# Kernel tuning notes

Hardware: AMD Instinct MI355X
Metric: run time of the kernel (lower is better)

## Reference

```python
import jax, jax.numpy as jnp
import numpy as np


def setup_inputs() -> dict:
    key = jax.random.key(0)
    k1, k2 = jax.random.split(key)
    B, D, H, W = 32, 64, 32, 32
    K = 1024
    z_e = jax.random.normal(k1, (B, D, H, W), dtype=jnp.float32)
    # original init: uniform(-1/K, 1/K); use same scale
    emb = jax.random.uniform(k2, (K, D), dtype=jnp.float32, minval=-1.0 / K, maxval=1.0 / K)
    return {"z_e": z_e, "emb": emb}


COMMITMENT_COST = 0.25


def reference(z_e, emb):
    # z_e: [B, D, H, W], emb: [K, D]
    B, D, H, W = z_e.shape
    K = emb.shape[0]
    z = jnp.transpose(z_e, (0, 2, 3, 1))           # [B, H, W, D]
    flat = z.reshape(-1, D)                        # [N, D]
    N = flat.shape[0]

    dist = (
        jnp.sum(flat * flat, axis=1, keepdims=True)
        + jnp.sum(emb * emb, axis=1)
        - 2.0 * flat @ emb.T
    )
    idx = jnp.argmin(dist, axis=1)                 # [N]
    encodings = jax.nn.one_hot(idx, K, dtype=flat.dtype)  # [N, K]
    z_q = (encodings @ emb).reshape(z.shape)       # [B, H, W, D]

    e_latent_loss = jnp.mean((jax.lax.stop_gradient(z_q) - z) ** 2)
    q_latent_loss = jnp.mean((z_q - jax.lax.stop_gradient(z)) ** 2)
    loss = q_latent_loss + COMMITMENT_COST * e_latent_loss

    # straight-through estimator
    z_st = z + jax.lax.stop_gradient(z_q - z)

    avg_probs = jnp.sum(encodings, axis=0) / jnp.float32(N)
    perplexity = jnp.exp(-jnp.sum(avg_probs * jnp.log(avg_probs + 1e-10)))

    return (jnp.transpose(z_st, (0, 3, 1, 2)), loss, perplexity, encodings)
```

## Files before the change

### kernel.cpp

```cpp
#include <hip/hip_runtime.h>
#include <stdint.h>
#include <math.h>

constexpr int Kk  = 1024;

constexpr int OUT0_N   = 32 * 64 * 1024;
constexpr int OUT_LOSS = OUT0_N;
constexpr int OUT_PERP = OUT0_N + 1;
constexpr int OUT_ENC  = OUT0_N + 2;

constexpr size_t WS_CNT = 0;
constexpr size_t WS_LP  = 4096;
constexpr size_t WS_MBN = 12288;
constexpr size_t WS_KEY = 16384;

typedef short bf16x8 __attribute__((ext_vector_type(8)));
typedef float f32x16 __attribute__((ext_vector_type(16)));

__device__ __forceinline__ float norm64v(const float4* __restrict__ p) {
#pragma clang fp contract(off)
    float tt[64];
#pragma unroll
    for (int q = 0; q < 16; ++q) {
        float4 v = p[q];
        tt[4 * q + 0] = v.x * v.x;
        tt[4 * q + 1] = v.y * v.y;
        tt[4 * q + 2] = v.z * v.z;
        tt[4 * q + 3] = v.w * v.w;
    }
    float r[8];
#pragma unroll
    for (int j = 0; j < 8; ++j) r[j] = tt[j];
#pragma unroll
    for (int i = 8; i < 64; i += 8)
#pragma unroll
        for (int j = 0; j < 8; ++j) r[j] += tt[i + j];
    return ((r[0] + r[1]) + (r[2] + r[3])) + ((r[4] + r[5]) + (r[6] + r[7]));
}

__device__ __forceinline__ uint32_t fsort(float f) {
    uint32_t b = __float_as_uint(f);
    return (b & 0x80000000u) ? ~b : (b | 0x80000000u);
}

__device__ __forceinline__ unsigned short f2bf(float f) {
    uint32_t u = __float_as_uint(f);
    uint32_t r = (u + 0x7fffu + ((u >> 16) & 1u)) >> 16;
    return (unsigned short)r;
}

__device__ __forceinline__ unsigned long long
exact_key(float A, const float* __restrict__ xr, const float* __restrict__ emb,
          uint32_t code) {
    const float* er = emb + (size_t)code * 64;
    float C = 0.f;
#pragma unroll
    for (int d = 0; d < 64; ++d) C = __builtin_fmaf(xr[d], er[d], C);
    float Bv = norm64v((const float4*)er);
    float s = A + Bv;
    float dist = __builtin_fmaf(-2.f, C, s);
    return ((unsigned long long)fsort(dist) << 32) | code;
}

__global__ __launch_bounds__(256, 4)
void dist_mfma(const float* __restrict__ z_e, const float* __restrict__ emb,
               unsigned long long* __restrict__ lockey,
               uint32_t* __restrict__ counts,
               float* __restrict__ maxbn,
               float* __restrict__ out) {
    __shared__ unsigned short xbf[128 * 64];
    __shared__ unsigned short ebf[128 * 64];
    __shared__ float Bn_s[128];
    __shared__ float xsqp[2][128];
    __shared__ float mbn_s;
    const int t = threadIdx.x, lane = t & 63, wv = t >> 6, g = lane >> 5;
    const int rg = blockIdx.x >> 3, cg = blockIdx.x & 7;
    const int n0 = rg * 128, b = n0 >> 10, hw0 = n0 & 1023;
    const float* zb = z_e + (size_t)b * 65536 + hw0;

    {
        int hwi = t & 127, d4g = t >> 7;
        float xq = 0.f;
#pragma unroll
        for (int it = 0; it < 8; ++it) {
            int dbase = (d4g + it * 2) * 4;
            float v0 = zb[(size_t)(dbase + 0) * 1024 + hwi];
            float v1 = zb[(size_t)(dbase + 1) * 1024 + hwi];
            float v2 = zb[(size_t)(dbase + 2) * 1024 + hwi];
            float v3 = zb[(size_t)(dbase + 3) * 1024 + hwi];
            xq = __builtin_fmaf(v0, v0, xq);
            xq = __builtin_fmaf(v1, v1, xq);
            xq = __builtin_fmaf(v2, v2, xq);
            xq = __builtin_fmaf(v3, v3, xq);
            ushort4 bv;
            bv.x = f2bf(v0); bv.y = f2bf(v1); bv.z = f2bf(v2); bv.w = f2bf(v3);
            *(ushort4*)((char*)xbf + hwi * 128 + ((dbase * 2) ^ ((hwi & 7) << 4))) = bv;
        }
        xsqp[d4g][hwi] = xq;
    }
    {
        const float4* ep = (const float4*)(emb + (size_t)cg * 8192);
#pragma unroll
        for (int it = 0; it < 8; ++it) {
            int j = t + it * 256;
            float4 v = ep[j];
            int code = j >> 4, q = j & 15;
            ushort4 bv;
            bv.x = f2bf(v.x); bv.y = f2bf(v.y); bv.z = f2bf(v.z); bv.w = f2bf(v.w);
            *(ushort4*)((char*)ebf + code * 128 + ((q * 8) ^ ((code & 7) << 4))) = bv;
        }
    }
    if (t < 128) Bn_s[t] = norm64v((const float4*)(emb + (size_t)(cg * 128 + t) * 64));
    if (blockIdx.x == 0) ((uint4*)counts)[t] = make_uint4(0u, 0u, 0u, 0u);
    __syncthreads();
    if (wv == 0) {
        float m = fmaxf(Bn_s[lane], Bn_s[lane + 64]);
#pragma unroll
        for (int s = 1; s < 64; s <<= 1) m = fmaxf(m, __shfl_xor(m, s, 64));
        if (lane == 0) { mbn_s = m; if (rg == 0) maxbn[cg] = m; }
    }
    __syncthreads();

    const int rowl = wv * 32 + (lane & 31);
    const float xsq = xsqp[0][rowl] + xsqp[1][rowl];
    const float margin = 0.017f * sqrtf(xsq * mbn_s) + 1.0e-4f;

    const int swz = (lane & 7) << 4;
    bf16x8 bfr[4];
    const char* xb = (const char*)xbf + rowl * 128;
#pragma unroll
    for (int s = 0; s < 4; ++s)
        bfr[s] = *(const bf16x8*)(xb + ((s * 32 + g * 16) ^ swz));
    const char* ebase = (const char*)ebf + (lane & 31) * 128;

    float4* encz = (float4*)(out + OUT_ENC) + (size_t)blockIdx.x * 4096;
    const float4 zero4 = make_float4(0.f, 0.f, 0.f, 0.f);

    float runmin = 3.4e38f;
#pragma unroll 1
    for (int tm = 0; tm < 4; ++tm) {
        encz[(size_t)(tm * 2 + 0) * 256 + t] = zero4;
        encz[(size_t)(tm * 2 + 1) * 256 + t] = zero4;
        const char* p = ebase + tm * 4096;
        f32x16 acc = {};
#pragma unroll
        for (int s = 0; s < 4; ++s)
            acc = __builtin_amdgcn_mfma_f32_32x32x16_bf16(
                *(const bf16x8*)(p + ((s * 32 + g * 16) ^ swz)), bfr[s], acc, 0, 0, 0);
#pragma unroll
        for (int r = 0; r < 16; ++r) {
            int cl = tm * 32 + (r & 3) + 8 * (r >> 2) + 4 * g;
            runmin = fminf(runmin, __builtin_fmaf(-2.f, acc[r], Bn_s[cl]));
        }
    }
    runmin = fminf(runmin, __shfl_xor(runmin, 32, 64));
    const float thr = runmin + margin;

    uint32_t cnt = 0, c0 = 0, c1 = 0, c2 = 0;
#pragma unroll 1
    for (int tm = 0; tm < 4; ++tm) {
        encz[(size_t)(8 + tm * 2 + 0) * 256 + t] = zero4;
        encz[(size_t)(8 + tm * 2 + 1) * 256 + t] = zero4;
        const char* p = ebase + tm * 4096;
        f32x16 acc = {};
#pragma unroll
        for (int s = 0; s < 4; ++s)
            acc = __builtin_amdgcn_mfma_f32_32x32x16_bf16(
                *(const bf16x8*)(p + ((s * 32 + g * 16) ^ swz)), bfr[s], acc, 0, 0, 0);
#pragma unroll
        for (int r = 0; r < 16; ++r) {
            int cl = tm * 32 + (r & 3) + 8 * (r >> 2) + 4 * g;
            float sv = __builtin_fmaf(-2.f, acc[r], Bn_s[cl]);
            if (sv <= thr) {
                uint32_t gc = (uint32_t)(cg * 128 + cl);
                if (cnt == 0u) c0 = gc; else if (cnt == 1u) c1 = gc; else if (cnt == 2u) c2 = gc;
                ++cnt;
            }
        }
    }
    uint32_t pc = __shfl_xor(cnt, 32, 64);
    uint32_t p0 = __shfl_xor(c0, 32, 64);
    uint32_t p1 = __shfl_xor(c1, 32, 64);
    uint32_t p2 = __shfl_xor(c2, 32, 64);
    if (lane < 32) {
        uint32_t tot = cnt + pc;
        uint32_t lo;
        if (tot > 3u || tot == 0u) {
            lo = 3u << 30;
        } else {
            uint32_t a0 = c0, a1 = c1, a2 = c2;
            if (cnt == 0u)      { a0 = p0; a1 = p1; a2 = p2; }
            else if (cnt == 1u) { a1 = p0; a2 = p1; }
            else if (cnt == 2u) { a2 = p0; }
            if (tot < 2u) a1 = 0u;
            if (tot < 3u) a2 = 0u;
            lo = ((tot - 1u) << 30) | (a0 & 1023u) | ((a1 & 1023u) << 10) | ((a2 & 1023u) << 20);
        }
        unsigned long long key = ((unsigned long long)__float_as_uint(runmin) << 32) | lo;
        lockey[(size_t)(n0 + rowl) * 8 + cg] = key;
    }
}

__global__ __launch_bounds__(256)
void finish_kernel(const float* __restrict__ z_e,
                   const float* __restrict__ emb,
                   const unsigned long long* __restrict__ lockey,
                   const float* __restrict__ maxbn,
                   uint32_t* __restrict__ counts,
                   double* __restrict__ lp,
                   float* __restrict__ out) {
    __shared__ float zs[32 * 68];
    __shared__ float arow[32];
    __shared__ uint32_t scode[32];
    __shared__ uint8_t ncarr[32];
    __shared__ unsigned long long pkey[32][6];
    __shared__ uint32_t pairbuf[192];
    __shared__ uint32_t ovfbuf[32];
    __shared__ uint32_t npairs, novf;
    __shared__ float mbg_s;
    __shared__ unsigned long long rbuf[4];
    __shared__ double lred[4];
    const int t = threadIdx.x, lane = t & 63, wv = t >> 6;
    const int n0 = blockIdx.x * 32;
    const int b = n0 >> 10, hw0 = n0 & 1023;
    const int hwi = t & 31, dg = t >> 5;
    const size_t base = (size_t)b * 65536 + (size_t)(dg * 8) * 1024 + hw0 + hwi;

    if (t == 0) {
        npairs = 0u; novf = 0u;
        float mb = maxbn[0];
#pragma unroll
        for (int i = 1; i < 8; ++i) mb = fmaxf(mb, maxbn[i]);
        mbg_s = mb;
    }

    float zreg[8];
#pragma unroll
    for (int k = 0; k < 8; ++k) zreg[k] = z_e[base + (size_t)k * 1024];
#pragma unroll
    for (int m = 0; m < 2; ++m)
        *(float4*)&zs[hwi * 68 + dg * 8 + 4 * m] =
            make_float4(zreg[4 * m], zreg[4 * m + 1], zreg[4 * m + 2], zreg[4 * m + 3]);
    __syncthreads();

    if (t < 32) {
        const unsigned long long* k8 = lockey + (size_t)(n0 + t) * 8;
        unsigned long long kws[8];
#pragma unroll
        for (int i = 0; i < 8; ++i) kws[i] = k8[i];
        float gmin = 3.4e38f;
#pragma unroll
        for (int i = 0; i < 8; ++i)
            gmin = fminf(gmin, __uint_as_float((uint32_t)(kws[i] >> 32)));
        float A = norm64v((const float4*)&zs[t * 68]);
        arow[t] = A;
        const float thr = gmin + 0.017f * sqrtf(A * mbg_s) + 1.0e-4f;

        int nc = 0; uint32_t cand[6]; bool ovf = false;
#pragma unroll
        for (int i = 0; i < 8; ++i) {
            float f = __uint_as_float((uint32_t)(kws[i] >> 32));
            if (f > thr) continue;
            uint32_t lo = (uint32_t)kws[i], cc = lo >> 30;
            if (cc == 3u) { ovf = true; }
            else {
#pragma unroll
                for (uint32_t q = 0; q < 3u; ++q)
                    if (q <= cc) {
                        if (nc < 6) cand[nc] = (lo >> (10u * q)) & 1023u;
                        ++nc;
                    }
            }
        }
        if (ovf || nc > 6 || nc == 0) {
            ncarr[t] = 255u;
            ovfbuf[atomicAdd(&novf, 1u)] = (uint32_t)t;
        } else if (nc == 1) {
            ncarr[t] = 1u;
            scode[t] = cand[0];
        } else {
            ncarr[t] = (uint8_t)nc;
            uint32_t bs = atomicAdd(&npairs, (uint32_t)nc);
#pragma unroll
            for (int q = 0; q < 6; ++q)
                if (q < nc)
                    pairbuf[bs + q] = ((uint32_t)t << 13) | ((uint32_t)q << 10) | cand[q];
        }
    }
    __syncthreads();

    for (uint32_t p = t; p < npairs; p += 256u) {
        uint32_t pk = pairbuf[p];
        int row = (int)(pk >> 13), slot = (int)((pk >> 10) & 7u);
        pkey[row][slot] = exact_key(arow[row], &zs[row * 68], emb, pk & 1023u);
    }
    __syncthreads();

    for (uint32_t o = 0; o < novf; ++o) {
        int row = (int)ovfbuf[o];
        const float* xr = &zs[row * 68];
        float A = arow[row];
        unsigned long long best = ~0ULL;
#pragma unroll 1
        for (int cq = 0; cq < 4; ++cq) {
            unsigned long long key = exact_key(A, xr, emb, (uint32_t)(t + cq * 256));
            best = (key < best) ? key : best;
        }
#pragma unroll
        for (int m = 1; m < 64; m <<= 1) {
            unsigned long long ok = __shfl_xor(best, m, 64);
            best = (ok < best) ? ok : best;
        }
        if (lane == 0) rbuf[wv] = best;
        __syncthreads();
        if (t == 0) {
            unsigned long long bb = rbuf[0];
#pragma unroll
            for (int w = 1; w < 4; ++w) bb = (rbuf[w] < bb) ? rbuf[w] : bb;
            scode[row] = (uint32_t)bb;
        }
        __syncthreads();
    }

    if (t < 32) {
        uint8_t nc = ncarr[t];
        if (nc >= 2u && nc != 255u) {
            unsigned long long bb = pkey[t][0];
#pragma unroll
            for (int q = 1; q < 6; ++q)
                if (q < (int)nc && pkey[t][q] < bb) bb = pkey[t][q];
            scode[t] = (uint32_t)bb;
        }
    }
    __syncthreads();

    if (t < 32) {
        uint32_t code = scode[t];
        atomicAdd(&counts[code], 1u);
        out[(size_t)OUT_ENC + (size_t)(n0 + t) * 1024 + code] = 1.0f;
    }

    {
        const uint32_t code = scode[hwi];
        const float4* er4 = (const float4*)(emb + (size_t)code * 64) + dg * 2;
        double ls = 0.0;
#pragma unroll
        for (int k4 = 0; k4 < 2; ++k4) {
            float4 e4 = er4[k4];
            float f0 = e4.x, f1 = e4.y, f2 = e4.z, f3 = e4.w;
            size_t off = base + (size_t)(k4 * 4) * 1024;
            {
                float z = zreg[k4 * 4 + 0]; float tt = f0 - z;
                out[off] = z + tt;              ls += (double)tt * (double)tt;
            }
            {
                float z = zreg[k4 * 4 + 1]; float tt = f1 - z;
                out[off + 1024] = z + tt;       ls += (double)tt * (double)tt;
            }
            {
                float z = zreg[k4 * 4 + 2]; float tt = f2 - z;
                out[off + 2048] = z + tt;       ls += (double)tt * (double)tt;
            }
            {
                float z = zreg[k4 * 4 + 3]; float tt = f3 - z;
                out[off + 3072] = z + tt;       ls += (double)tt * (double)tt;
            }
        }
#pragma unroll
        for (int m = 32; m >= 1; m >>= 1) ls += __shfl_down(ls, m, 64);
        if ((t & 63) == 0) lred[t >> 6] = ls;
    }
    __syncthreads();
    if (t == 0) lp[blockIdx.x] = lred[0] + lred[1] + lred[2] + lred[3];
}

__global__ void scalar_kernel(const uint32_t* __restrict__ counts,
                              const double* __restrict__ lp,
                              float* __restrict__ out) {
    __shared__ double redl[4], redh[4];
    const int t = threadIdx.x;
    double ls = 0.0;
    for (int i = t; i < 1024; i += 256) ls += lp[i];
    double h = 0.0;
    for (int i = t; i < Kk; i += 256) {
        double p = (double)counts[i] * (1.0 / 32768.0);
        h += p * log(p + 1e-10);
    }
#pragma unroll
    for (int m = 32; m >= 1; m >>= 1) { ls += __shfl_down(ls, m, 64); h += __shfl_down(h, m, 64); }
    if ((t & 63) == 0) { redl[t >> 6] = ls; redh[t >> 6] = h; }
    __syncthreads();
    if (t == 0) {
        double L = redl[0] + redl[1] + redl[2] + redl[3];
        double H = redh[0] + redh[1] + redh[2] + redh[3];
        out[OUT_PERP] = (float)exp(-H);
        float m32 = (float)(L * (1.0 / 2097152.0));
        out[OUT_LOSS] = m32 + 0.25f * m32;
    }
}

extern "C" void kernel_launch(void* const* d_in, const int* in_sizes, int n_in,
                              void* d_out, int out_size, void* d_ws, size_t ws_size,
                              hipStream_t stream) {
    const float* z_e = (const float*)d_in[0];
    const float* emb = (const float*)d_in[1];
    float* out = (float*)d_out;
    char* ws = (char*)d_ws;

    uint32_t* counts = (uint32_t*)(ws + WS_CNT);
    double*   lp     = (double*)(ws + WS_LP);
    float*    mbn    = (float*)(ws + WS_MBN);
    unsigned long long* lockey = (unsigned long long*)(ws + WS_KEY);

    dist_mfma<<<2048, 256, 0, stream>>>(z_e, emb, lockey, counts, mbn, out);
    finish_kernel<<<1024, 256, 0, stream>>>(z_e, emb, lockey, mbn, counts, lp, out);
    scalar_kernel<<<1, 256, 0, stream>>>(counts, lp, out);
}
```

Before: 199.6 us.

## Precompute codebook norms in a prepass and simplify candidate keys

Adds a small norms kernel that computes all codebook squared norms and per-block maxima once, and zeroes the counts buffer. The distance kernel now reads those norms instead of recomputing them per block. It also loads z rows straight into MFMA fragment registers rather than staging them through shared memory, and writes only the 32-bit candidate list without the running minimum. The finish kernel drops the threshold filter, re-checks every candidate exactly using the precomputed norms, and allows up to 24 per row. The trade-off is an extra launch and more exact checks per row, in exchange for less redundant norm work and less shared memory in the distance kernel.

```diff
diff --git a/kernel.cpp b/kernel.cpp
--- a/kernel.cpp
+++ b/kernel.cpp
@@ -11,8 +11,9 @@
 
 constexpr size_t WS_CNT = 0;
 constexpr size_t WS_LP  = 4096;
-constexpr size_t WS_MBN = 12288;
-constexpr size_t WS_KEY = 16384;
+constexpr size_t WS_BN  = 12288;
+constexpr size_t WS_MBN = 16384;
+constexpr size_t WS_KEY = 16400;
 
 typedef short bf16x8 __attribute__((ext_vector_type(8)));
 typedef float f32x16 __attribute__((ext_vector_type(16)));
@@ -50,54 +51,45 @@
 }
 
 __device__ __forceinline__ unsigned long long
-exact_key(float A, const float* __restrict__ xr, const float* __restrict__ emb,
-          uint32_t code) {
+exact_key_bn(float A, const float* __restrict__ xr, const float* __restrict__ emb,
+             const float* __restrict__ Bn_g, uint32_t code) {
     const float* er = emb + (size_t)code * 64;
     float C = 0.f;
 #pragma unroll
     for (int d = 0; d < 64; ++d) C = __builtin_fmaf(xr[d], er[d], C);
-    float Bv = norm64v((const float4*)er);
-    float s = A + Bv;
+    float s = A + Bn_g[code];
     float dist = __builtin_fmaf(-2.f, C, s);
     return ((unsigned long long)fsort(dist) << 32) | code;
 }
 
+__global__ __launch_bounds__(256)
+void norms_kernel(const float* __restrict__ emb, float* __restrict__ Bn_g,
+                  float* __restrict__ maxbn, uint32_t* __restrict__ counts) {
+    __shared__ float wred[4];
+    const int t = threadIdx.x, lane = t & 63, wv = t >> 6;
+    const int code = blockIdx.x * 256 + t;
+    float nn = norm64v((const float4*)(emb + (size_t)code * 64));
+    Bn_g[code] = nn;
+    if (blockIdx.x == 0) ((uint4*)counts)[t] = make_uint4(0u, 0u, 0u, 0u);
+    float mx = nn;
+#pragma unroll
+    for (int m = 1; m < 64; m <<= 1) mx = fmaxf(mx, __shfl_xor(mx, m, 64));
+    if (lane == 0) wred[wv] = mx;
+    __syncthreads();
+    if (t == 0) maxbn[blockIdx.x] = fmaxf(fmaxf(wred[0], wred[1]), fmaxf(wred[2], wred[3]));
+}
+
 __global__ __launch_bounds__(256, 4)
 void dist_mfma(const float* __restrict__ z_e, const float* __restrict__ emb,
-               unsigned long long* __restrict__ lockey,
-               uint32_t* __restrict__ counts,
-               float* __restrict__ maxbn,
-               float* __restrict__ out) {
-    __shared__ unsigned short xbf[128 * 64];
+               const float* __restrict__ Bn_g, const float* __restrict__ maxbn,
+               uint32_t* __restrict__ lockey, float* __restrict__ out) {
     __shared__ unsigned short ebf[128 * 64];
     __shared__ float Bn_s[128];
-    __shared__ float xsqp[2][128];
-    __shared__ float mbn_s;
     const int t = threadIdx.x, lane = t & 63, wv = t >> 6, g = lane >> 5;
     const int rg = blockIdx.x >> 3, cg = blockIdx.x & 7;
     const int n0 = rg * 128, b = n0 >> 10, hw0 = n0 & 1023;
     const float* zb = z_e + (size_t)b * 65536 + hw0;
 
-    {
-        int hwi = t & 127, d4g = t >> 7;
-        float xq = 0.f;
-#pragma unroll
-        for (int it = 0; it < 8; ++it) {
-            int dbase = (d4g + it * 2) * 4;
-            float v0 = zb[(size_t)(dbase + 0) * 1024 + hwi];
-            float v1 = zb[(size_t)(dbase + 1) * 1024 + hwi];
-            float v2 = zb[(size_t)(dbase + 2) * 1024 + hwi];
-            float v3 = zb[(size_t)(dbase + 3) * 1024 + hwi];
-            xq = __builtin_fmaf(v0, v0, xq);
-            xq = __builtin_fmaf(v1, v1, xq);
-            xq = __builtin_fmaf(v2, v2, xq);
-            xq = __builtin_fmaf(v3, v3, xq);
-            ushort4 bv;
-            bv.x = f2bf(v0); bv.y = f2bf(v1); bv.z = f2bf(v2); bv.w = f2bf(v3);
-            *(ushort4*)((char*)xbf + hwi * 128 + ((dbase * 2) ^ ((hwi & 7) << 4))) = bv;
-        }
-        xsqp[d4g][hwi] = xq;
-    }
     {
         const float4* ep = (const float4*)(emb + (size_t)cg * 8192);
 #pragma unroll
@@ -110,27 +102,29 @@
             *(ushort4*)((char*)ebf + code * 128 + ((q * 8) ^ ((code & 7) << 4))) = bv;
         }
     }
-    if (t < 128) Bn_s[t] = norm64v((const float4*)(emb + (size_t)(cg * 128 + t) * 64));
-    if (blockIdx.x == 0) ((uint4*)counts)[t] = make_uint4(0u, 0u, 0u, 0u);
-    __syncthreads();
-    if (wv == 0) {
-        float m = fmaxf(Bn_s[lane], Bn_s[lane + 64]);
-#pragma unroll
-        for (int s = 1; s < 64; s <<= 1) m = fmaxf(m, __shfl_xor(m, s, 64));
-        if (lane == 0) { mbn_s = m; if (rg == 0) maxbn[cg] = m; }
-    }
-    __syncthreads();
+    if (t < 128) Bn_s[t] = Bn_g[cg * 128 + t];
 
     const int rowl = wv * 32 + (lane & 31);
-    const float xsq = xsqp[0][rowl] + xsqp[1][rowl];
-    const float margin = 0.017f * sqrtf(xsq * mbn_s) + 1.0e-4f;
+    float xsq = 0.f;
+    bf16x8 bfr[4];
+#pragma unroll
+    for (int s = 0; s < 4; ++s) {
+        bf16x8 f;
+#pragma unroll
+        for (int e = 0; e < 8; ++e) {
+            int d = s * 16 + g * 8 + e;
+            float x = zb[(size_t)d * 1024 + rowl];
+            xsq = __builtin_fmaf(x, x, xsq);
+            f[e] = (short)f2bf(x);
+        }
+        bfr[s] = f;
+    }
+    xsq += __shfl_xor(xsq, 32, 64);
+    const float mbn = fmaxf(fmaxf(maxbn[0], maxbn[1]), fmaxf(maxbn[2], maxbn[3]));
+    const float margin = 0.017f * sqrtf(xsq * mbn) + 1.0e-4f;
+    __syncthreads();
 
     const int swz = (lane & 7) << 4;
-    bf16x8 bfr[4];
-    const char* xb = (const char*)xbf + rowl * 128;
-#pragma unroll
-    for (int s = 0; s < 4; ++s)
-        bfr[s] = *(const bf16x8*)(xb + ((s * 32 + g * 16) ^ swz));
     const char* ebase = (const char*)ebf + (lane & 31) * 128;
 
     float4* encz = (float4*)(out + OUT_ENC) + (size_t)blockIdx.x * 4096;
@@ -196,28 +190,24 @@
             if (tot < 3u) a2 = 0u;
             lo = ((tot - 1u) << 30) | (a0 & 1023u) | ((a1 & 1023u) << 10) | ((a2 & 1023u) << 20);
         }
-        unsigned long long key = ((unsigned long long)__float_as_uint(runmin) << 32) | lo;
-        lockey[(size_t)(n0 + rowl) * 8 + cg] = key;
+        lockey[(size_t)(n0 + rowl) * 8 + cg] = lo;
     }
 }
 
 __global__ __launch_bounds__(256)
-void finish_kernel(const float* __restrict__ z_e,
-                   const float* __restrict__ emb,
-                   const unsigned long long* __restrict__ lockey,
-                   const float* __restrict__ maxbn,
-                   uint32_t* __restrict__ counts,
-                   double* __restrict__ lp,
+void finish_kernel(const float* __restrict__ z_e, const float* __restrict__ emb,
+                   const uint32_t* __restrict__ lockey,
+                   const float* __restrict__ Bn_g,
+                   uint32_t* __restrict__ counts, double* __restrict__ lp,
                    float* __restrict__ out) {
     __shared__ float zs[32 * 68];
     __shared__ float arow[32];
     __shared__ uint32_t scode[32];
     __shared__ uint8_t ncarr[32];
-    __shared__ unsigned long long pkey[32][6];
-    __shared__ uint32_t pairbuf[192];
+    __shared__ unsigned long long pkey[32][24];
+    __shared__ uint32_t pairbuf[32 * 24];
     __shared__ uint32_t ovfbuf[32];
-    __shared__ uint32_t npairs, novf;
-    __shared__ float mbg_s;
+    __shared__ uint32_t novf;
     __shared__ unsigned long long rbuf[4];
     __shared__ double lred[4];
     const int t = threadIdx.x, lane = t & 63, wv = t >> 6;
@@ -226,13 +216,7 @@
     const int hwi = t & 31, dg = t >> 5;
     const size_t base = (size_t)b * 65536 + (size_t)(dg * 8) * 1024 + hw0 + hwi;
 
-    if (t == 0) {
-        npairs = 0u; novf = 0u;
-        float mb = maxbn[0];
-#pragma unroll
-        for (int i = 1; i < 8; ++i) mb = fmaxf(mb, maxbn[i]);
-        mbg_s = mb;
-    }
+    if (t == 0) novf = 0u;
 
     float zreg[8];
 #pragma unroll
@@ -244,55 +228,39 @@
     __syncthreads();
 
     if (t < 32) {
-        const unsigned long long* k8 = lockey + (size_t)(n0 + t) * 8;
-        unsigned long long kws[8];
-#pragma unroll
-        for (int i = 0; i < 8; ++i) kws[i] = k8[i];
-        float gmin = 3.4e38f;
-#pragma unroll
-        for (int i = 0; i < 8; ++i)
-            gmin = fminf(gmin, __uint_as_float((uint32_t)(kws[i] >> 32)));
+        const uint32_t* k8 = lockey + (size_t)(n0 + t) * 8;
+        int nc = 0; bool ovf = false;
+#pragma unroll
+        for (int i = 0; i < 8; ++i) {
+            uint32_t lo = k8[i];
+            uint32_t cc = lo >> 30;
+            if (cc == 3u) { ovf = true; }
+            else {
+#pragma unroll
+                for (uint32_t q = 0; q < 3u; ++q)
+                    if (q <= cc) { pairbuf[t * 24 + nc] = (lo >> (10u * q)) & 1023u; ++nc; }
+            }
+        }
         float A = norm64v((const float4*)&zs[t * 68]);
         arow[t] = A;
-        const float thr = gmin + 0.017f * sqrtf(A * mbg_s) + 1.0e-4f;
-
-        int nc = 0; uint32_t cand[6]; bool ovf = false;
-#pragma unroll
-        for (int i = 0; i < 8; ++i) {
-            float f = __uint_as_float((uint32_t)(kws[i] >> 32));
-            if (f > thr) continue;
-            uint32_t lo = (uint32_t)kws[i], cc = lo >> 30;
-            if (cc == 3u) { ovf = true; }
-            else {
-#pragma unroll
-                for (uint32_t q = 0; q < 3u; ++q)
-                    if (q <= cc) {
-                        if (nc < 6) cand[nc] = (lo >> (10u * q)) & 1023u;
-                        ++nc;
-                    }
-            }
-        }
-        if (ovf || nc > 6 || nc == 0) {
+        if (ovf || nc == 0) {
             ncarr[t] = 255u;
             ovfbuf[atomicAdd(&novf, 1u)] = (uint32_t)t;
         } else if (nc == 1) {
             ncarr[t] = 1u;
-            scode[t] = cand[0];
+            scode[t] = pairbuf[t * 24];
         } else {
             ncarr[t] = (uint8_t)nc;
-            uint32_t bs = atomicAdd(&npairs, (uint32_t)nc);
-#pragma unroll
-            for (int q = 0; q < 6; ++q)
-                if (q < nc)
-                    pairbuf[bs + q] = ((uint32_t)t << 13) | ((uint32_t)q << 10) | cand[q];
-        }
-    }
-    __syncthreads();
-
-    for (uint32_t p = t; p < npairs; p += 256u) {
-        uint32_t pk = pairbuf[p];
-        int row = (int)(pk >> 13), slot = (int)((pk >> 10) & 7u);
-        pkey[row][slot] = exact_key(arow[row], &zs[row * 68], emb, pk & 1023u);
+        }
+    }
+    __syncthreads();
+
+#pragma unroll 1
+    for (int p = t; p < 32 * 24; p += 256) {
+        int row = p / 24, slot = p - row * 24;
+        uint8_t nc = ncarr[row];
+        if (nc >= 2u && nc != 255u && slot < (int)nc)
+            pkey[row][slot] = exact_key_bn(arow[row], &zs[row * 68], emb, Bn_g, pairbuf[p]);
     }
     __syncthreads();
 
@@ -303,7 +271,7 @@
         unsigned long long best = ~0ULL;
 #pragma unroll 1
         for (int cq = 0; cq < 4; ++cq) {
-            unsigned long long key = exact_key(A, xr, emb, (uint32_t)(t + cq * 256));
+            unsigned long long key = exact_key_bn(A, xr, emb, Bn_g, (uint32_t)(t + cq * 256));
             best = (key < best) ? key : best;
         }
 #pragma unroll
@@ -326,9 +294,9 @@
         uint8_t nc = ncarr[t];
         if (nc >= 2u && nc != 255u) {
             unsigned long long bb = pkey[t][0];
-#pragma unroll
-            for (int q = 1; q < 6; ++q)
-                if (q < (int)nc && pkey[t][q] < bb) bb = pkey[t][q];
+#pragma unroll 1
+            for (int q = 1; q < (int)nc; ++q)
+                if (pkey[t][q] < bb) bb = pkey[t][q];
             scode[t] = (uint32_t)bb;
         }
     }
@@ -409,10 +377,12 @@
 
     uint32_t* counts = (uint32_t*)(ws + WS_CNT);
     double*   lp     = (double*)(ws + WS_LP);
+    float*    Bn_g   = (float*)(ws + WS_BN);
     float*    mbn    = (float*)(ws + WS_MBN);
-    unsigned long long* lockey = (unsigned long long*)(ws + WS_KEY);
-
-    dist_mfma<<<2048, 256, 0, stream>>>(z_e, emb, lockey, counts, mbn, out);
-    finish_kernel<<<1024, 256, 0, stream>>>(z_e, emb, lockey, mbn, counts, lp, out);
+    uint32_t* lockey = (uint32_t*)(ws + WS_KEY);
+
+    norms_kernel<<<4, 256, 0, stream>>>(emb, Bn_g, mbn, counts);
+    dist_mfma<<<2048, 256, 0, stream>>>(z_e, emb, Bn_g, mbn, lockey, out);
+    finish_kernel<<<1024, 256, 0, stream>>>(z_e, emb, lockey, Bn_g, counts, lp, out);
     scalar_kernel<<<1, 256, 0, stream>>>(counts, lp, out);
 }
```

After: 311.1 us. +55.9%, slower.
